# Optimization experiments

Measured on AMD Instinct MI355X. Metric: run time of the kernel, lower is better.

Reference implementation:

```python
import jax, jax.numpy as jnp
import numpy as np

N = 250000   # num nodes
E = 250000   # num edges (tree: ~one parent per node)
D = 128      # embed_size
H = 256      # MLP hidden
HOPS = 3


def _mlp(x, w1, b1, w2, b2):
    # Sequential(Linear, ReLU, Linear, ReLU, Dropout(eval=identity))
    return jax.nn.relu(jnp.dot(jax.nn.relu(jnp.dot(x, w1) + b1), w2) + b2)


def _scatter_mean(src, idx, n):
    s = jax.ops.segment_sum(src, idx, num_segments=n)
    c = jax.ops.segment_sum(jnp.ones((src.shape[0],), src.dtype), idx, num_segments=n)
    return s / jnp.maximum(c, 1.0)[:, None]


def setup_inputs() -> dict:
    key = jax.random.key(0)
    ks = jax.random.split(key, 32)
    u = lambda k, shp: jax.random.uniform(k, shp, jnp.float32, -0.1, 0.1)
    inp = {
        "batch_token": jax.random.normal(ks[0], (N, D), jnp.float32),
        "self_idx_batch": jax.random.randint(ks[1], (E,), 0, N),
        "parent_idx_batch": jax.random.randint(ks[2], (E,), 0, N),
        "root_mask": (jax.random.uniform(ks[3], (N,)) < 0.01).astype(jnp.float32),
        "leaf_mask": (jax.random.uniform(ks[4], (N,)) < 0.3).astype(jnp.float32),
        "start_token": jax.random.normal(ks[5], (D,), jnp.float32),
        "end_token": jax.random.normal(ks[6], (D,), jnp.float32),
        # MLP_V: D -> H -> D
        "Vw1": u(ks[7], (D, H)), "Vb1": u(ks[8], (H,)), "Vw2": u(ks[9], (H, D)), "Vb2": u(ks[10], (D,)),
        # MLP_E: 1 -> H -> D
        "Ew1": u(ks[11], (1, H)), "Eb1": u(ks[12], (H,)), "Ew2": u(ks[13], (H, D)), "Eb2": u(ks[14], (D,)),
        # MLP_p: 3D -> H -> D
        "Pw1": u(ks[15], (3 * D, H)), "Pb1": u(ks[16], (H,)), "Pw2": u(ks[17], (H, D)), "Pb2": u(ks[18], (D,)),
        # MLP_c: 3D -> H -> D
        "Cw1": u(ks[19], (3 * D, H)), "Cb1": u(ks[20], (H,)), "Cw2": u(ks[21], (H, D)), "Cb2": u(ks[22], (D,)),
        # MLP_aggr: 3D -> H -> D
        "Aw1": u(ks[23], (3 * D, H)), "Ab1": u(ks[24], (H,)), "Aw2": u(ks[25], (H, D)), "Ab2": u(ks[26], (D,)),
    }
    return inp


def reference(batch_token, self_idx_batch, parent_idx_batch, root_mask, leaf_mask,
              start_token, end_token,
              Vw1, Vb1, Vw2, Vb2,
              Ew1, Eb1, Ew2, Eb2,
              Pw1, Pb1, Pw2, Pb2,
              Cw1, Cb1, Cw2, Cb2,
              Aw1, Ab1, Aw2, Ab2):
    n = batch_token.shape[0]
    edge_in = _mlp(jnp.ones((1, 1), batch_token.dtype), Ew1, Eb1, Ew2, Eb2)   # [1,D]
    edge_out = _mlp(jnp.zeros((1, 1), batch_token.dtype), Ew1, Eb1, Ew2, Eb2)  # [1,D]
    e = self_idx_batch.shape[0]
    edge_in = jnp.broadcast_to(edge_in, (e, edge_in.shape[1]))
    edge_out = jnp.broadcast_to(edge_out, (e, edge_out.shape[1]))

    hidden = _mlp(batch_token, Vw1, Vb1, Vw2, Vb2)  # [N,D]
    for _ in range(HOPS):
        node_self = hidden[self_idx_batch]      # [E,D] gather
        node_parent = hidden[parent_idx_batch]  # [E,D] gather
        inp_parent = jnp.concatenate([node_parent, node_self, edge_out], axis=-1)  # [E,3D]
        inp_child = jnp.concatenate([node_self, node_parent, edge_in], axis=-1)    # [E,3D]
        S_p = _mlp(inp_parent, Pw1, Pb1, Pw2, Pb2)
        S_c = _mlp(inp_child, Cw1, Cb1, Cw2, Cb2)
        S_p = _scatter_mean(S_p, self_idx_batch, n)
        S_c = _scatter_mean(S_c, parent_idx_batch, n)
        S_p = S_p + root_mask[:, None] * start_token
        S_c = S_c + leaf_mask[:, None] * end_token
        x_aggr = jnp.concatenate([hidden, S_p, S_c], axis=-1)  # [N,3D]
        hidden = hidden + _mlp(x_aggr, Aw1, Ab1, Aw2, Ab2)
    return hidden
```

## Files before the change

### kernel.cpp

```cpp
#include <hip/hip_runtime.h>

typedef __attribute__((ext_vector_type(8))) short short8;
typedef __attribute__((ext_vector_type(4))) float f32x4;

#define DD 128
#define HH 256

__device__ __forceinline__ unsigned short f2bf(float f) {
  unsigned int u = __float_as_uint(f);
  u += 0x7fffu + ((u >> 16) & 1u);
  return (unsigned short)(u >> 16);
}
__device__ __forceinline__ float bf2f(unsigned short s) {
  return __uint_as_float(((unsigned int)s) << 16);
}
__device__ __forceinline__ f32x4 mfma16(short8 a, short8 b, f32x4 c) {
  return __builtin_amdgcn_mfma_f32_16x16x32_bf16(a, b, c, 0, 0, 0);
}

__global__ void wconv(const float* __restrict__ src, unsigned short* __restrict__ dst,
                      int K, int Nout, int kswap) {
  int id = blockIdx.x * 256 + threadIdx.x;
  if (id >= K * Nout) return;
  int n = id / K, k = id - n * K;
  int ks = k + kswap; if (ks >= K) ks -= K;
  dst[n * K + k] = f2bf(src[(size_t)ks * Nout + n]);
}

__global__ void prep_bias(const float* __restrict__ Ew1, const float* __restrict__ Eb1,
                          const float* __restrict__ Ew2, const float* __restrict__ Eb2,
                          const float* __restrict__ Pw1, const float* __restrict__ Pb1,
                          const float* __restrict__ Cw1, const float* __restrict__ Cb1,
                          float* __restrict__ b1P, float* __restrict__ b1C) {
  __shared__ float h1[HH], h0[HH], ein[DD], eout[DD];
  int t = threadIdx.x;
  h1[t] = fmaxf(Ew1[t] + Eb1[t], 0.f);
  h0[t] = fmaxf(Eb1[t], 0.f);
  __syncthreads();
  if (t < DD) {
    float s1 = Eb2[t], s0 = Eb2[t];
    for (int j = 0; j < HH; ++j) { s1 += h1[j] * Ew2[j * DD + t]; s0 += h0[j] * Ew2[j * DD + t]; }
    ein[t]  = fmaxf(s1, 0.f);
    eout[t] = fmaxf(s0, 0.f);
  }
  __syncthreads();
  float bp = Pb1[t], bc = Cb1[t];
  for (int d = 0; d < DD; ++d) {
    bp += eout[d] * Pw1[(size_t)(256 + d) * HH + t];
    bc += ein[d]  * Cw1[(size_t)(256 + d) * HH + t];
  }
  b1P[t] = bp; b1C[t] = bc;
}

__global__ void count_k(const int* __restrict__ selfI, const int* __restrict__ parI,
                        int* degP, int* degC, int E) {
  int id = blockIdx.x * 256 + threadIdx.x;
  if (id < E) { atomicAdd(&degP[selfI[id]], 1); atomicAdd(&degC[parI[id]], 1); }
}

__global__ void scan1(const int* __restrict__ src, int* __restrict__ dst,
                      int* __restrict__ part, int n) {
  __shared__ int sh[256];
  int t = threadIdx.x;
  int base = blockIdx.x * 1024 + t * 4;
  int v0 = base + 0 < n ? src[base + 0] : 0;
  int v1 = base + 1 < n ? src[base + 1] : 0;
  int v2 = base + 2 < n ? src[base + 2] : 0;
  int v3 = base + 3 < n ? src[base + 3] : 0;
  int tsum = v0 + v1 + v2 + v3;
  sh[t] = tsum;
  __syncthreads();
  for (int off = 1; off < 256; off <<= 1) {
    int y = (t >= off) ? sh[t - off] : 0;
    __syncthreads();
    if (t >= off) sh[t] += y;
    __syncthreads();
  }
  int ex = sh[t] - tsum;
  if (base + 0 < n) dst[base + 0] = ex;
  if (base + 1 < n) dst[base + 1] = ex + v0;
  if (base + 2 < n) dst[base + 2] = ex + v0 + v1;
  if (base + 3 < n) dst[base + 3] = ex + v0 + v1 + v2;
  if (t == 255) part[blockIdx.x] = sh[255];
}

__global__ void scan2(int* __restrict__ part, int m) {
  __shared__ int sh[256];
  int t = threadIdx.x;
  int carry = 0;
  for (int base = 0; base < m; base += 256) {
    int v = (base + t < m) ? part[base + t] : 0;
    sh[t] = v;
    __syncthreads();
    for (int off = 1; off < 256; off <<= 1) {
      int y = (t >= off) ? sh[t - off] : 0;
      __syncthreads();
      if (t >= off) sh[t] += y;
      __syncthreads();
    }
    if (base + t < m) part[base + t] = carry + sh[t] - v;
    int tot = sh[255];
    __syncthreads();
    carry += tot;
  }
}

__global__ void scan3(int* __restrict__ dst, const int* __restrict__ part, int n) {
  int i = blockIdx.x * 256 + threadIdx.x;
  if (i < n) dst[i] += part[i >> 10];
}

__global__ void copy2(const int* __restrict__ a, int* __restrict__ b,
                      const int* __restrict__ c, int* __restrict__ d, int n) {
  int i = blockIdx.x * 256 + threadIdx.x;
  if (i < n) { b[i] = a[i]; d[i] = c[i]; }
}

__global__ void pos_k(const int* __restrict__ selfI, const int* __restrict__ parI,
                      int* curP, int* curC, int* posP, int* posC, int E) {
  int e = blockIdx.x * 256 + threadIdx.x;
  if (e < E) {
    posP[e] = atomicAdd(&curP[selfI[e]], 1);
    posC[e] = atomicAdd(&curC[parI[e]], 1);
  }
}

__global__ __launch_bounds__(512, 4) void v_kernel(
    const float* __restrict__ x, const unsigned short* __restrict__ W1t,
    const unsigned short* __restrict__ W2t, const float* __restrict__ b1,
    const float* __restrict__ b2, float* __restrict__ hidden, int n) {
  __shared__ __align__(16) unsigned short A[64 * 136];
  __shared__ __align__(16) unsigned short O1[64 * 264];
  int t = threadIdx.x;
  int w = t >> 6, lane = t & 63, ln = lane & 15, quad = lane >> 4, qo = quad * 8;
  long tile0 = (long)blockIdx.x * 64;
  int rl = t >> 3, part = t & 7;
  int c0 = part * 16;
  long gr = tile0 + rl;
  const float* src = x + (size_t)(gr < n ? gr : 0) * DD + c0;
  unsigned short* arow = A + rl * 136 + c0;
#pragma unroll
  for (int i = 0; i < 4; ++i) {
    float4 v = *(const float4*)(src + i * 4);
    *(ushort4*)(arow + i * 4) = make_ushort4(f2bf(v.x), f2bf(v.y), f2bf(v.z), f2bf(v.w));
  }
  __syncthreads();
  f32x4 acc[4][2];
#pragma unroll
  for (int m = 0; m < 4; ++m) {
    acc[m][0] = {0.f, 0.f, 0.f, 0.f}; acc[m][1] = {0.f, 0.f, 0.f, 0.f};
  }
#pragma unroll
  for (int kt = 0; kt < 4; ++kt) {
    short8 a[4];
#pragma unroll
    for (int m = 0; m < 4; ++m)
      a[m] = *(const short8*)(A + (m * 16 + ln) * 136 + kt * 32 + qo);
#pragma unroll
    for (int nn = 0; nn < 2; ++nn) {
      short8 b = *(const short8*)(W1t + (size_t)(w * 32 + nn * 16 + ln) * 128 + kt * 32 + qo);
#pragma unroll
      for (int m = 0; m < 4; ++m) acc[m][nn] = mfma16(a[m], b, acc[m][nn]);
    }
  }
#pragma unroll
  for (int nn = 0; nn < 2; ++nn) {
    int col = w * 32 + nn * 16 + ln;
    float bb = b1[col];
#pragma unroll
    for (int m = 0; m < 4; ++m)
#pragma unroll
      for (int r = 0; r < 4; ++r)
        O1[(m * 16 + quad * 4 + r) * 264 + col] = f2bf(fmaxf(acc[m][nn][r] + bb, 0.f));
  }
  __syncthreads();
  f32x4 acc2[4];
#pragma unroll
  for (int m = 0; m < 4; ++m) acc2[m] = {0.f, 0.f, 0.f, 0.f};
#pragma unroll
  for (int kt = 0; kt < 8; ++kt) {
    short8 b = *(const short8*)(W2t + (size_t)(w * 16 + ln) * 256 + kt * 32 + qo);
#pragma unroll
    for (int m = 0; m < 4; ++m) {
      short8 a = *(const short8*)(O1 + (m * 16 + ln) * 264 + kt * 32 + qo);
      acc2[m] = mfma16(a, b, acc2[m]);
    }
  }
  {
    int col = w * 16 + ln;
    float bb = b2[col];
#pragma unroll
    for (int m = 0; m < 4; ++m)
#pragma unroll
      for (int r = 0; r < 4; ++r) {
        long gr2 = tile0 + m * 16 + quad * 4 + r;
        if (gr2 < n) hidden[gr2 * DD + col] = fmaxf(acc2[m][r] + bb, 0.f);
      }
  }
}

__global__ __launch_bounds__(512, 4) void edge_kernel(
    const float* __restrict__ hidden, const int* __restrict__ selfI, const int* __restrict__ parI,
    const int* __restrict__ posP, const int* __restrict__ posC,
    const unsigned short* __restrict__ Pw1t, const unsigned short* __restrict__ Pw2t,
    const unsigned short* __restrict__ Cw1t, const unsigned short* __restrict__ Cw2t,
    const float* __restrict__ b1P, const float* __restrict__ b1C,
    const float* __restrict__ b2P, const float* __restrict__ b2C,
    unsigned short* __restrict__ SpE, unsigned short* __restrict__ ScE, int E) {
  __shared__ __align__(16) unsigned short A[64 * 264];
  __shared__ __align__(16) unsigned short O1[64 * 264];
  int t = threadIdx.x;
  int w = t >> 6, lane = t & 63, ln = lane & 15, quad = lane >> 4, qo = quad * 8;
  long tile0 = (long)blockIdx.x * 64;
  int rl = t >> 3, part = t & 7;
  long ge = tile0 + rl;
  bool vrow = ge < E;
  int si = vrow ? selfI[ge] : 0;
  int pi = vrow ? parI[ge] : 0;
  const float* src = (part < 4) ? (hidden + (size_t)si * DD + part * 32)
                                : (hidden + (size_t)pi * DD + (part - 4) * 32);
  unsigned short* dstA = A + rl * 264 + part * 32;
#pragma unroll
  for (int i = 0; i < 8; ++i) {
    float4 v = *(const float4*)(src + i * 4);
    *(ushort4*)(dstA + i * 4) = make_ushort4(f2bf(v.x), f2bf(v.y), f2bf(v.z), f2bf(v.w));
  }
  __syncthreads();

  f32x4 accP[4][2], accC[4][2];
#pragma unroll
  for (int m = 0; m < 4; ++m) {
    accP[m][0] = {0.f, 0.f, 0.f, 0.f}; accP[m][1] = {0.f, 0.f, 0.f, 0.f};
    accC[m][0] = {0.f, 0.f, 0.f, 0.f}; accC[m][1] = {0.f, 0.f, 0.f, 0.f};
  }
#pragma unroll
  for (int kt = 0; kt < 8; ++kt) {
    short8 a[4];
#pragma unroll
    for (int m = 0; m < 4; ++m)
      a[m] = *(const short8*)(A + (m * 16 + ln) * 264 + kt * 32 + qo);
#pragma unroll
    for (int nn = 0; nn < 2; ++nn) {
      short8 bp = *(const short8*)(Pw1t + (size_t)(w * 32 + nn * 16 + ln) * 256 + kt * 32 + qo);
      short8 bc = *(const short8*)(Cw1t + (size_t)(w * 32 + nn * 16 + ln) * 256 + kt * 32 + qo);
#pragma unroll
      for (int m = 0; m < 4; ++m) {
        accP[m][nn] = mfma16(a[m], bp, accP[m][nn]);
        accC[m][nn] = mfma16(a[m], bc, accC[m][nn]);
      }
    }
  }
  __syncthreads();

#pragma unroll
  for (int mlp = 0; mlp < 2; ++mlp) {
    const unsigned short* W2t = mlp ? Cw2t : Pw2t;
    const float* b1 = mlp ? b1C : b1P;
    const float* b2 = mlp ? b2C : b2P;
    unsigned short* Sout = mlp ? ScE : SpE;
    const int* pos = mlp ? posC : posP;
#pragma unroll
    for (int nn = 0; nn < 2; ++nn) {
      int col = w * 32 + nn * 16 + ln;
      float bb = b1[col];
#pragma unroll
      for (int m = 0; m < 4; ++m)
#pragma unroll
        for (int r = 0; r < 4; ++r) {
          float v = mlp ? accC[m][nn][r] : accP[m][nn][r];
          O1[(m * 16 + quad * 4 + r) * 264 + col] = f2bf(fmaxf(v + bb, 0.f));
        }
    }
    __syncthreads();
    f32x4 acc2[4];
#pragma unroll
    for (int m = 0; m < 4; ++m) acc2[m] = {0.f, 0.f, 0.f, 0.f};
#pragma unroll
    for (int kt = 0; kt < 8; ++kt) {
      short8 b = *(const short8*)(W2t + (size_t)(w * 16 + ln) * 256 + kt * 32 + qo);
#pragma unroll
      for (int m = 0; m < 4; ++m) {
        short8 a = *(const short8*)(O1 + (m * 16 + ln) * 264 + kt * 32 + qo);
        acc2[m] = mfma16(a, b, acc2[m]);
      }
    }
    __syncthreads();
    {
      int col = w * 16 + ln;
      float bb = b2[col];
#pragma unroll
      for (int m = 0; m < 4; ++m)
#pragma unroll
        for (int r = 0; r < 4; ++r)
          O1[(m * 16 + quad * 4 + r) * 264 + col] = f2bf(fmaxf(acc2[m][r] + bb, 0.f));
    }
    __syncthreads();
    if (vrow) {
      int dpos = pos[ge];
      const unsigned short* srow = O1 + rl * 264 + part * 16;
      ushort4* dst = (ushort4*)(Sout + (size_t)dpos * DD + part * 16);
#pragma unroll
      for (int i = 0; i < 4; ++i) dst[i] = *(const ushort4*)(srow + i * 4);
    }
    __syncthreads();
  }
}

__global__ __launch_bounds__(512, 4) void node_kernel(
    float* __restrict__ hidden,
    const unsigned short* __restrict__ SpE, const unsigned short* __restrict__ ScE,
    const int* __restrict__ offP, const int* __restrict__ degP,
    const int* __restrict__ offC, const int* __restrict__ degC,
    const float* __restrict__ rootM, const float* __restrict__ leafM,
    const float* __restrict__ startT, const float* __restrict__ endT,
    const unsigned short* __restrict__ W1t, const unsigned short* __restrict__ W2t,
    const float* __restrict__ b1, const float* __restrict__ b2, int n) {
  __shared__ __align__(16) unsigned short A[64 * 392];
  int t = threadIdx.x;
  int w = t >> 6, lane = t & 63, ln = lane & 15, quad = lane >> 4, qo = quad * 8;
  long tile0 = (long)blockIdx.x * 64;
  int rl = t >> 3, part = t & 7;
  int c0 = part * 16;
  long gr = tile0 + rl;
  long g = (gr < n) ? gr : 0;
  unsigned short* arow = A + rl * 392;
  {
    const float* hrow = hidden + (size_t)g * DD + c0;
#pragma unroll
    for (int i = 0; i < 4; ++i) {
      float4 h = *(const float4*)(hrow + i * 4);
      *(ushort4*)(arow + c0 + i * 4) = make_ushort4(f2bf(h.x), f2bf(h.y), f2bf(h.z), f2bf(h.w));
    }
  }
  {
    int off = offP[g], dg = degP[g];
    float s[16];
#pragma unroll
    for (int i = 0; i < 16; ++i) s[i] = 0.f;
    for (int j = 0; j < dg; ++j) {
      const unsigned short* rr = SpE + (size_t)(off + j) * DD + c0;
#pragma unroll
      for (int i = 0; i < 4; ++i) {
        ushort4 u = *(const ushort4*)(rr + i * 4);
        s[i * 4 + 0] += bf2f(u.x); s[i * 4 + 1] += bf2f(u.y);
        s[i * 4 + 2] += bf2f(u.z); s[i * 4 + 3] += bf2f(u.w);
      }
    }
    float ip = 1.f / fmaxf((float)dg, 1.f);
    float rm = rootM[g];
#pragma unroll
    for (int i = 0; i < 4; ++i) {
      float4 st = *(const float4*)(startT + c0 + i * 4);
      *(ushort4*)(arow + 128 + c0 + i * 4) = make_ushort4(
          f2bf(s[i * 4 + 0] * ip + rm * st.x), f2bf(s[i * 4 + 1] * ip + rm * st.y),
          f2bf(s[i * 4 + 2] * ip + rm * st.z), f2bf(s[i * 4 + 3] * ip + rm * st.w));
    }
  }
  {
    int off = offC[g], dg = degC[g];
    float s[16];
#pragma unroll
    for (int i = 0; i < 16; ++i) s[i] = 0.f;
    for (int j = 0; j < dg; ++j) {
      const unsigned short* rr = ScE + (size_t)(off + j) * DD + c0;
#pragma unroll
      for (int i = 0; i < 4; ++i) {
        ushort4 u = *(const ushort4*)(rr + i * 4);
        s[i * 4 + 0] += bf2f(u.x); s[i * 4 + 1] += bf2f(u.y);
        s[i * 4 + 2] += bf2f(u.z); s[i * 4 + 3] += bf2f(u.w);
      }
    }
    float ic = 1.f / fmaxf((float)dg, 1.f);
    float lm = leafM[g];
#pragma unroll
    for (int i = 0; i < 4; ++i) {
      float4 et = *(const float4*)(endT + c0 + i * 4);
      *(ushort4*)(arow + 256 + c0 + i * 4) = make_ushort4(
          f2bf(s[i * 4 + 0] * ic + lm * et.x), f2bf(s[i * 4 + 1] * ic + lm * et.y),
          f2bf(s[i * 4 + 2] * ic + lm * et.z), f2bf(s[i * 4 + 3] * ic + lm * et.w));
    }
  }
  __syncthreads();
  f32x4 acc[4][2];
#pragma unroll
  for (int m = 0; m < 4; ++m) {
    acc[m][0] = {0.f, 0.f, 0.f, 0.f}; acc[m][1] = {0.f, 0.f, 0.f, 0.f};
  }
#pragma unroll
  for (int kt = 0; kt < 12; ++kt) {
    short8 a[4];
#pragma unroll
    for (int m = 0; m < 4; ++m)
      a[m] = *(const short8*)(A + (m * 16 + ln) * 392 + kt * 32 + qo);
#pragma unroll
    for (int nn = 0; nn < 2; ++nn) {
      short8 b = *(const short8*)(W1t + (size_t)(w * 32 + nn * 16 + ln) * 384 + kt * 32 + qo);
#pragma unroll
      for (int m = 0; m < 4; ++m) acc[m][nn] = mfma16(a[m], b, acc[m][nn]);
    }
  }
  __syncthreads();
#pragma unroll
  for (int nn = 0; nn < 2; ++nn) {
    int col = w * 32 + nn * 16 + ln;
    float bb = b1[col];
#pragma unroll
    for (int m = 0; m < 4; ++m)
#pragma unroll
      for (int r = 0; r < 4; ++r)
        A[(m * 16 + quad * 4 + r) * 392 + col] = f2bf(fmaxf(acc[m][nn][r] + bb, 0.f));
  }
  __syncthreads();
  f32x4 acc2[4];
#pragma unroll
  for (int m = 0; m < 4; ++m) acc2[m] = {0.f, 0.f, 0.f, 0.f};
#pragma unroll
  for (int kt = 0; kt < 8; ++kt) {
    short8 b = *(const short8*)(W2t + (size_t)(w * 16 + ln) * 256 + kt * 32 + qo);
#pragma unroll
    for (int m = 0; m < 4; ++m) {
      short8 a = *(const short8*)(A + (m * 16 + ln) * 392 + kt * 32 + qo);
      acc2[m] = mfma16(a, b, acc2[m]);
    }
  }
  __syncthreads();
  {
    int col = w * 16 + ln;
    float bb = b2[col];
#pragma unroll
    for (int m = 0; m < 4; ++m)
#pragma unroll
      for (int r = 0; r < 4; ++r)
        ((float*)(A + (size_t)(m * 16 + quad * 4 + r) * 392))[col] =
            fmaxf(acc2[m][r] + bb, 0.f);
  }
  __syncthreads();
  if (gr < n) {
    const float* F = (const float*)(A + (size_t)rl * 392);
    float* hrow = hidden + (size_t)gr * DD + c0;
#pragma unroll
    for (int i = 0; i < 4; ++i) {
      float4 v = *(const float4*)(F + c0 + i * 4);
      float4 h = *(const float4*)(hrow + i * 4);
      h.x += v.x; h.y += v.y; h.z += v.z; h.w += v.w;
      *(float4*)(hrow + i * 4) = h;
    }
  }
}

extern "C" void kernel_launch(void* const* d_in, const int* in_sizes, int n_in,
                              void* d_out, int out_size, void* d_ws, size_t ws_size,
                              hipStream_t stream) {
  const float* batch  = (const float*)d_in[0];
  const int*   selfI  = (const int*)d_in[1];
  const int*   parI   = (const int*)d_in[2];
  const float* rootM  = (const float*)d_in[3];
  const float* leafM  = (const float*)d_in[4];
  const float* startT = (const float*)d_in[5];
  const float* endT   = (const float*)d_in[6];
  const float* Vw1 = (const float*)d_in[7],  *Vb1 = (const float*)d_in[8];
  const float* Vw2 = (const float*)d_in[9],  *Vb2 = (const float*)d_in[10];
  const float* Ew1 = (const float*)d_in[11], *Eb1 = (const float*)d_in[12];
  const float* Ew2 = (const float*)d_in[13], *Eb2 = (const float*)d_in[14];
  const float* Pw1 = (const float*)d_in[15], *Pb1 = (const float*)d_in[16];
  const float* Pw2 = (const float*)d_in[17], *Pb2 = (const float*)d_in[18];
  const float* Cw1 = (const float*)d_in[19], *Cb1 = (const float*)d_in[20];
  const float* Cw2 = (const float*)d_in[21], *Cb2 = (const float*)d_in[22];
  const float* Aw1 = (const float*)d_in[23], *Ab1 = (const float*)d_in[24];
  const float* Aw2 = (const float*)d_in[25], *Ab2 = (const float*)d_in[26];

  const int N = in_sizes[3];
  const int E = in_sizes[1];
  float* out = (float*)d_out;

  char* p = (char*)d_ws;
  auto nxt = [&](size_t sz) { char* r = p; p += (sz + 255) & ~(size_t)255; return r; };
  unsigned short* SpE = (unsigned short*)nxt((size_t)E * DD * 2);
  unsigned short* ScE = (unsigned short*)nxt((size_t)E * DD * 2);
  int* degP = (int*)nxt((size_t)N * 4);
  int* degC = (int*)nxt((size_t)N * 4);
  int* offP = (int*)nxt((size_t)N * 4);
  int* offC = (int*)nxt((size_t)N * 4);
  int* curP = (int*)nxt((size_t)N * 4);
  int* curC = (int*)nxt((size_t)N * 4);
  int* posP = (int*)nxt((size_t)E * 4);
  int* posC = (int*)nxt((size_t)E * 4);
  int* partA = (int*)nxt(4096);
  int* partB = (int*)nxt(4096);
  unsigned short* Vw1t = (unsigned short*)nxt((size_t)128 * 256 * 2);
  unsigned short* Vw2t = (unsigned short*)nxt((size_t)256 * 128 * 2);
  unsigned short* Pw1t = (unsigned short*)nxt((size_t)256 * 256 * 2);
  unsigned short* Pw2t = (unsigned short*)nxt((size_t)256 * 128 * 2);
  unsigned short* Cw1t = (unsigned short*)nxt((size_t)256 * 256 * 2);
  unsigned short* Cw2t = (unsigned short*)nxt((size_t)256 * 128 * 2);
  unsigned short* Aw1t = (unsigned short*)nxt((size_t)384 * 256 * 2);
  unsigned short* Aw2t = (unsigned short*)nxt((size_t)256 * 128 * 2);
  float* b1P = (float*)nxt(256 * 4);
  float* b1C = (float*)nxt(256 * 4);

  hipMemsetAsync(degP, 0, (size_t)N * 4, stream);
  hipMemsetAsync(degC, 0, (size_t)N * 4, stream);

  auto blk = [](int total) { return dim3((total + 255) / 256); };
  wconv<<<blk(128 * 256), 256, 0, stream>>>(Vw1, Vw1t, 128, 256, 0);
  wconv<<<blk(256 * 128), 256, 0, stream>>>(Vw2, Vw2t, 256, 128, 0);
  wconv<<<blk(256 * 256), 256, 0, stream>>>(Pw1, Pw1t, 256, 256, 128);
  wconv<<<blk(256 * 128), 256, 0, stream>>>(Pw2, Pw2t, 256, 128, 0);
  wconv<<<blk(256 * 256), 256, 0, stream>>>(Cw1, Cw1t, 256, 256, 0);
  wconv<<<blk(256 * 128), 256, 0, stream>>>(Cw2, Cw2t, 256, 128, 0);
  wconv<<<blk(384 * 256), 256, 0, stream>>>(Aw1, Aw1t, 384, 256, 0);
  wconv<<<blk(256 * 128), 256, 0, stream>>>(Aw2, Aw2t, 256, 128, 0);

  prep_bias<<<1, 256, 0, stream>>>(Ew1, Eb1, Ew2, Eb2, Pw1, Pb1, Cw1, Cb1, b1P, b1C);
  count_k<<<blk(E), 256, 0, stream>>>(selfI, parI, degP, degC, E);

  int NB = (N + 1023) / 1024;
  scan1<<<NB, 256, 0, stream>>>(degP, offP, partA, N);
  scan1<<<NB, 256, 0, stream>>>(degC, offC, partB, N);
  scan2<<<1, 256, 0, stream>>>(partA, NB);
  scan2<<<1, 256, 0, stream>>>(partB, NB);
  scan3<<<blk(N), 256, 0, stream>>>(offP, partA, N);
  scan3<<<blk(N), 256, 0, stream>>>(offC, partB, N);
  copy2<<<blk(N), 256, 0, stream>>>(offP, curP, offC, curC, N);
  pos_k<<<blk(E), 256, 0, stream>>>(selfI, parI, curP, curC, posP, posC, E);

  dim3 gN((N + 63) / 64), gE((E + 63) / 64);
  v_kernel<<<gN, 512, 0, stream>>>(batch, Vw1t, Vw2t, Vb1, Vb2, out, N);

  for (int hop = 0; hop < 3; ++hop) {
    edge_kernel<<<gE, 512, 0, stream>>>(out, selfI, parI, posP, posC,
                                        Pw1t, Pw2t, Cw1t, Cw2t, b1P, b1C, Pb2, Cb2,
                                        SpE, ScE, E);
    node_kernel<<<gN, 512, 0, stream>>>(out, SpE, ScE, offP, degP, offC, degC,
                                        rootM, leafM, startT, endT,
                                        Aw1t, Aw2t, Ab1, Ab2, N);
  }
}
```

Before: 1.834 ms.

## Shrink MLP tiles to 32 rows with 4 waves and scatter edge outputs directly

All three MLP kernels now process 32 rows per block with 256 threads (4 waves), so each wave covers 64 hidden columns and 32 output columns, cutting LDS per block and doubling grid size. The edge kernel preloads the scatter positions into shared memory and writes second-layer outputs straight from registers to their sorted positions. This removes the LDS staging round trip and several barriers. In exchange it issues scalar 2-byte global stores instead of vectorized row copies, and weight fragments are reloaded per 32-row tile, doubling weight traffic.

```diff
diff --git a/kernel.cpp b/kernel.cpp
--- a/kernel.cpp
+++ b/kernel.cpp
@@ -125,15 +125,15 @@
   }
 }
 
-__global__ __launch_bounds__(512, 4) void v_kernel(
+__global__ __launch_bounds__(256, 4) void v_kernel(
     const float* __restrict__ x, const unsigned short* __restrict__ W1t,
     const unsigned short* __restrict__ W2t, const float* __restrict__ b1,
     const float* __restrict__ b2, float* __restrict__ hidden, int n) {
-  __shared__ __align__(16) unsigned short A[64 * 136];
-  __shared__ __align__(16) unsigned short O1[64 * 264];
+  __shared__ __align__(16) unsigned short A[32 * 136];
+  __shared__ __align__(16) unsigned short O1[32 * 264];
   int t = threadIdx.x;
   int w = t >> 6, lane = t & 63, ln = lane & 15, quad = lane >> 4, qo = quad * 8;
-  long tile0 = (long)blockIdx.x * 64;
+  long tile0 = (long)blockIdx.x * 32;
   int rl = t >> 3, part = t & 7;
   int c0 = part * 16;
   long gr = tile0 + rl;
@@ -145,61 +145,66 @@
     *(ushort4*)(arow + i * 4) = make_ushort4(f2bf(v.x), f2bf(v.y), f2bf(v.z), f2bf(v.w));
   }
   __syncthreads();
-  f32x4 acc[4][2];
-#pragma unroll
-  for (int m = 0; m < 4; ++m) {
-    acc[m][0] = {0.f, 0.f, 0.f, 0.f}; acc[m][1] = {0.f, 0.f, 0.f, 0.f};
-  }
+  f32x4 acc[2][4];
+#pragma unroll
+  for (int m = 0; m < 2; ++m)
+#pragma unroll
+    for (int nn = 0; nn < 4; ++nn) acc[m][nn] = {0.f, 0.f, 0.f, 0.f};
 #pragma unroll
   for (int kt = 0; kt < 4; ++kt) {
-    short8 a[4];
-#pragma unroll
-    for (int m = 0; m < 4; ++m)
+    short8 a[2];
+#pragma unroll
+    for (int m = 0; m < 2; ++m)
       a[m] = *(const short8*)(A + (m * 16 + ln) * 136 + kt * 32 + qo);
 #pragma unroll
+    for (int nn = 0; nn < 4; ++nn) {
+      short8 b = *(const short8*)(W1t + (size_t)(w * 64 + nn * 16 + ln) * 128 + kt * 32 + qo);
+#pragma unroll
+      for (int m = 0; m < 2; ++m) acc[m][nn] = mfma16(a[m], b, acc[m][nn]);
+    }
+  }
+#pragma unroll
+  for (int nn = 0; nn < 4; ++nn) {
+    int col = w * 64 + nn * 16 + ln;
+    float bb = b1[col];
+#pragma unroll
+    for (int m = 0; m < 2; ++m)
+#pragma unroll
+      for (int r = 0; r < 4; ++r)
+        O1[(m * 16 + quad * 4 + r) * 264 + col] = f2bf(fmaxf(acc[m][nn][r] + bb, 0.f));
+  }
+  __syncthreads();
+  f32x4 acc2[2][2];
+#pragma unroll
+  for (int m = 0; m < 2; ++m) { acc2[m][0] = {0.f, 0.f, 0.f, 0.f}; acc2[m][1] = {0.f, 0.f, 0.f, 0.f}; }
+#pragma unroll
+  for (int kt = 0; kt < 8; ++kt) {
+    short8 a2[2];
+#pragma unroll
+    for (int m = 0; m < 2; ++m)
+      a2[m] = *(const short8*)(O1 + (m * 16 + ln) * 264 + kt * 32 + qo);
+#pragma unroll
     for (int nn = 0; nn < 2; ++nn) {
-      short8 b = *(const short8*)(W1t + (size_t)(w * 32 + nn * 16 + ln) * 128 + kt * 32 + qo);
-#pragma unroll
-      for (int m = 0; m < 4; ++m) acc[m][nn] = mfma16(a[m], b, acc[m][nn]);
+      short8 b = *(const short8*)(W2t + (size_t)(w * 32 + nn * 16 + ln) * 256 + kt * 32 + qo);
+#pragma unroll
+      for (int m = 0; m < 2; ++m) acc2[m][nn] = mfma16(a2[m], b, acc2[m][nn]);
     }
   }
 #pragma unroll
   for (int nn = 0; nn < 2; ++nn) {
     int col = w * 32 + nn * 16 + ln;
-    float bb = b1[col];
-#pragma unroll
-    for (int m = 0; m < 4; ++m)
-#pragma unroll
-      for (int r = 0; r < 4; ++r)
-        O1[(m * 16 + quad * 4 + r) * 264 + col] = f2bf(fmaxf(acc[m][nn][r] + bb, 0.f));
-  }
-  __syncthreads();
-  f32x4 acc2[4];
-#pragma unroll
-  for (int m = 0; m < 4; ++m) acc2[m] = {0.f, 0.f, 0.f, 0.f};
-#pragma unroll
-  for (int kt = 0; kt < 8; ++kt) {
-    short8 b = *(const short8*)(W2t + (size_t)(w * 16 + ln) * 256 + kt * 32 + qo);
-#pragma unroll
-    for (int m = 0; m < 4; ++m) {
-      short8 a = *(const short8*)(O1 + (m * 16 + ln) * 264 + kt * 32 + qo);
-      acc2[m] = mfma16(a, b, acc2[m]);
-    }
-  }
-  {
-    int col = w * 16 + ln;
     float bb = b2[col];
 #pragma unroll
-    for (int m = 0; m < 4; ++m)
+    for (int m = 0; m < 2; ++m)
 #pragma unroll
       for (int r = 0; r < 4; ++r) {
         long gr2 = tile0 + m * 16 + quad * 4 + r;
-        if (gr2 < n) hidden[gr2 * DD + col] = fmaxf(acc2[m][r] + bb, 0.f);
+        if (gr2 < n) hidden[gr2 * DD + col] = fmaxf(acc2[m][nn][r] + bb, 0.f);
       }
   }
 }
 
-__global__ __launch_bounds__(512, 4) void edge_kernel(
+__global__ __launch_bounds__(256, 4) void edge_kernel(
     const float* __restrict__ hidden, const int* __restrict__ selfI, const int* __restrict__ parI,
     const int* __restrict__ posP, const int* __restrict__ posC,
     const unsigned short* __restrict__ Pw1t, const unsigned short* __restrict__ Pw2t,
@@ -207,16 +212,24 @@
     const float* __restrict__ b1P, const float* __restrict__ b1C,
     const float* __restrict__ b2P, const float* __restrict__ b2C,
     unsigned short* __restrict__ SpE, unsigned short* __restrict__ ScE, int E) {
-  __shared__ __align__(16) unsigned short A[64 * 264];
-  __shared__ __align__(16) unsigned short O1[64 * 264];
+  __shared__ __align__(16) unsigned short A[32 * 264];
+  __shared__ __align__(16) unsigned short O1[32 * 264];
+  __shared__ int posS[2][32];
   int t = threadIdx.x;
   int w = t >> 6, lane = t & 63, ln = lane & 15, quad = lane >> 4, qo = quad * 8;
-  long tile0 = (long)blockIdx.x * 64;
+  long tile0 = (long)blockIdx.x * 32;
   int rl = t >> 3, part = t & 7;
   long ge = tile0 + rl;
   bool vrow = ge < E;
   int si = vrow ? selfI[ge] : 0;
   int pi = vrow ? parI[ge] : 0;
+  if (t < 64) {
+    int rr = t & 31;
+    long gg = tile0 + rr;
+    int v = 0;
+    if (gg < E) v = (t < 32) ? posP[gg] : posC[gg];
+    posS[t >> 5][rr] = v;
+  }
   const float* src = (part < 4) ? (hidden + (size_t)si * DD + part * 32)
                                 : (hidden + (size_t)pi * DD + (part - 4) * 32);
   unsigned short* dstA = A + rl * 264 + part * 32;
@@ -227,30 +240,31 @@
   }
   __syncthreads();
 
-  f32x4 accP[4][2], accC[4][2];
-#pragma unroll
-  for (int m = 0; m < 4; ++m) {
-    accP[m][0] = {0.f, 0.f, 0.f, 0.f}; accP[m][1] = {0.f, 0.f, 0.f, 0.f};
-    accC[m][0] = {0.f, 0.f, 0.f, 0.f}; accC[m][1] = {0.f, 0.f, 0.f, 0.f};
-  }
+  f32x4 accP[2][4], accC[2][4];
+#pragma unroll
+  for (int m = 0; m < 2; ++m)
+#pragma unroll
+    for (int nn = 0; nn < 4; ++nn) {
+      accP[m][nn] = {0.f, 0.f, 0.f, 0.f};
+      accC[m][nn] = {0.f, 0.f, 0.f, 0.f};
+    }
 #pragma unroll
   for (int kt = 0; kt < 8; ++kt) {
-    short8 a[4];
-#pragma unroll
-    for (int m = 0; m < 4; ++m)
+    short8 a[2];
+#pragma unroll
+    for (int m = 0; m < 2; ++m)
       a[m] = *(const short8*)(A + (m * 16 + ln) * 264 + kt * 32 + qo);
 #pragma unroll
-    for (int nn = 0; nn < 2; ++nn) {
-      short8 bp = *(const short8*)(Pw1t + (size_t)(w * 32 + nn * 16 + ln) * 256 + kt * 32 + qo);
-      short8 bc = *(const short8*)(Cw1t + (size_t)(w * 32 + nn * 16 + ln) * 256 + kt * 32 + qo);
-#pragma unroll
-      for (int m = 0; m < 4; ++m) {
+    for (int nn = 0; nn < 4; ++nn) {
+      short8 bp = *(const short8*)(Pw1t + (size_t)(w * 64 + nn * 16 + ln) * 256 + kt * 32 + qo);
+      short8 bc = *(const short8*)(Cw1t + (size_t)(w * 64 + nn * 16 + ln) * 256 + kt * 32 + qo);
+#pragma unroll
+      for (int m = 0; m < 2; ++m) {
         accP[m][nn] = mfma16(a[m], bp, accP[m][nn]);
         accC[m][nn] = mfma16(a[m], bc, accC[m][nn]);
       }
     }
   }
-  __syncthreads();
 
 #pragma unroll
   for (int mlp = 0; mlp < 2; ++mlp) {
@@ -258,13 +272,13 @@
     const float* b1 = mlp ? b1C : b1P;
     const float* b2 = mlp ? b2C : b2P;
     unsigned short* Sout = mlp ? ScE : SpE;
-    const int* pos = mlp ? posC : posP;
-#pragma unroll
-    for (int nn = 0; nn < 2; ++nn) {
-      int col = w * 32 + nn * 16 + ln;
+    if (mlp) __syncthreads();
+#pragma unroll
+    for (int nn = 0; nn < 4; ++nn) {
+      int col = w * 64 + nn * 16 + ln;
       float bb = b1[col];
 #pragma unroll
-      for (int m = 0; m < 4; ++m)
+      for (int m = 0; m < 2; ++m)
 #pragma unroll
         for (int r = 0; r < 4; ++r) {
           float v = mlp ? accC[m][nn][r] : accP[m][nn][r];
@@ -272,41 +286,41 @@
         }
     }
     __syncthreads();
-    f32x4 acc2[4];
-#pragma unroll
-    for (int m = 0; m < 4; ++m) acc2[m] = {0.f, 0.f, 0.f, 0.f};
+    f32x4 acc2[2][2];
+#pragma unroll
+    for (int m = 0; m < 2; ++m) { acc2[m][0] = {0.f, 0.f, 0.f, 0.f}; acc2[m][1] = {0.f, 0.f, 0.f, 0.f}; }
 #pragma unroll
     for (int kt = 0; kt < 8; ++kt) {
-      short8 b = *(const short8*)(W2t + (size_t)(w * 16 + ln) * 256 + kt * 32 + qo);
-#pragma unroll
-      for (int m = 0; m < 4; ++m) {
-        short8 a = *(const short8*)(O1 + (m * 16 + ln) * 264 + kt * 32 + qo);
-        acc2[m] = mfma16(a, b, acc2[m]);
+      short8 a2[2];
+#pragma unroll
+      for (int m = 0; m < 2; ++m)
+        a2[m] = *(const short8*)(O1 + (m * 16 + ln) * 264 + kt * 32 + qo);
+#pragma unroll
+      for (int nn = 0; nn < 2; ++nn) {
+        short8 b = *(const short8*)(W2t + (size_t)(w * 32 + nn * 16 + ln) * 256 + kt * 32 + qo);
+#pragma unroll
+        for (int m = 0; m < 2; ++m) acc2[m][nn] = mfma16(a2[m], b, acc2[m][nn]);
       }
     }
-    __syncthreads();
-    {
-      int col = w * 16 + ln;
+#pragma unroll
+    for (int nn = 0; nn < 2; ++nn) {
+      int col = w * 32 + nn * 16 + ln;
       float bb = b2[col];
 #pragma unroll
-      for (int m = 0; m < 4; ++m)
-#pragma unroll
-        for (int r = 0; r < 4; ++r)
-          O1[(m * 16 + quad * 4 + r) * 264 + col] = f2bf(fmaxf(acc2[m][r] + bb, 0.f));
-    }
-    __syncthreads();
-    if (vrow) {
-      int dpos = pos[ge];
-      const unsigned short* srow = O1 + rl * 264 + part * 16;
-      ushort4* dst = (ushort4*)(Sout + (size_t)dpos * DD + part * 16);
-#pragma unroll
-      for (int i = 0; i < 4; ++i) dst[i] = *(const ushort4*)(srow + i * 4);
-    }
-    __syncthreads();
-  }
-}
-
-__global__ __launch_bounds__(512, 4) void node_kernel(
+      for (int m = 0; m < 2; ++m)
+#pragma unroll
+        for (int r = 0; r < 4; ++r) {
+          int row = m * 16 + quad * 4 + r;
+          if (tile0 + row < E) {
+            int dpos = posS[mlp][row];
+            Sout[(size_t)dpos * DD + col] = f2bf(fmaxf(acc2[m][nn][r] + bb, 0.f));
+          }
+        }
+    }
+  }
+}
+
+__global__ __launch_bounds__(256, 4) void node_kernel(
     float* __restrict__ hidden,
     const unsigned short* __restrict__ SpE, const unsigned short* __restrict__ ScE,
     const int* __restrict__ offP, const int* __restrict__ degP,
@@ -315,10 +329,10 @@
     const float* __restrict__ startT, const float* __restrict__ endT,
     const unsigned short* __restrict__ W1t, const unsigned short* __restrict__ W2t,
     const float* __restrict__ b1, const float* __restrict__ b2, int n) {
-  __shared__ __align__(16) unsigned short A[64 * 392];
+  __shared__ __align__(16) unsigned short A[32 * 392];
   int t = threadIdx.x;
   int w = t >> 6, lane = t & 63, ln = lane & 15, quad = lane >> 4, qo = quad * 8;
-  long tile0 = (long)blockIdx.x * 64;
+  long tile0 = (long)blockIdx.x * 32;
   int rl = t >> 3, part = t & 7;
   int c0 = part * 16;
   long gr = tile0 + rl;
@@ -381,58 +395,63 @@
     }
   }
   __syncthreads();
-  f32x4 acc[4][2];
-#pragma unroll
-  for (int m = 0; m < 4; ++m) {
-    acc[m][0] = {0.f, 0.f, 0.f, 0.f}; acc[m][1] = {0.f, 0.f, 0.f, 0.f};
-  }
+  f32x4 acc[2][4];
+#pragma unroll
+  for (int m = 0; m < 2; ++m)
+#pragma unroll
+    for (int nn = 0; nn < 4; ++nn) acc[m][nn] = {0.f, 0.f, 0.f, 0.f};
 #pragma unroll
   for (int kt = 0; kt < 12; ++kt) {
-    short8 a[4];
-#pragma unroll
-    for (int m = 0; m < 4; ++m)
+    short8 a[2];
+#pragma unroll
+    for (int m = 0; m < 2; ++m)
       a[m] = *(const short8*)(A + (m * 16 + ln) * 392 + kt * 32 + qo);
 #pragma unroll
+    for (int nn = 0; nn < 4; ++nn) {
+      short8 b = *(const short8*)(W1t + (size_t)(w * 64 + nn * 16 + ln) * 384 + kt * 32 + qo);
+#pragma unroll
+      for (int m = 0; m < 2; ++m) acc[m][nn] = mfma16(a[m], b, acc[m][nn]);
+    }
+  }
+  __syncthreads();
+#pragma unroll
+  for (int nn = 0; nn < 4; ++nn) {
+    int col = w * 64 + nn * 16 + ln;
+    float bb = b1[col];
+#pragma unroll
+    for (int m = 0; m < 2; ++m)
+#pragma unroll
+      for (int r = 0; r < 4; ++r)
+        A[(m * 16 + quad * 4 + r) * 392 + col] = f2bf(fmaxf(acc[m][nn][r] + bb, 0.f));
+  }
+  __syncthreads();
+  f32x4 acc2[2][2];
+#pragma unroll
+  for (int m = 0; m < 2; ++m) { acc2[m][0] = {0.f, 0.f, 0.f, 0.f}; acc2[m][1] = {0.f, 0.f, 0.f, 0.f}; }
+#pragma unroll
+  for (int kt = 0; kt < 8; ++kt) {
+    short8 a2[2];
+#pragma unroll
+    for (int m = 0; m < 2; ++m)
+      a2[m] = *(const short8*)(A + (m * 16 + ln) * 392 + kt * 32 + qo);
+#pragma unroll
     for (int nn = 0; nn < 2; ++nn) {
-      short8 b = *(const short8*)(W1t + (size_t)(w * 32 + nn * 16 + ln) * 384 + kt * 32 + qo);
-#pragma unroll
-      for (int m = 0; m < 4; ++m) acc[m][nn] = mfma16(a[m], b, acc[m][nn]);
+      short8 b = *(const short8*)(W2t + (size_t)(w * 32 + nn * 16 + ln) * 256 + kt * 32 + qo);
+#pragma unroll
+      for (int m = 0; m < 2; ++m) acc2[m][nn] = mfma16(a2[m], b, acc2[m][nn]);
     }
   }
   __syncthreads();
 #pragma unroll
   for (int nn = 0; nn < 2; ++nn) {
     int col = w * 32 + nn * 16 + ln;
-    float bb = b1[col];
-#pragma unroll
-    for (int m = 0; m < 4; ++m)
-#pragma unroll
-      for (int r = 0; r < 4; ++r)
-        A[(m * 16 + quad * 4 + r) * 392 + col] = f2bf(fmaxf(acc[m][nn][r] + bb, 0.f));
-  }
-  __syncthreads();
-  f32x4 acc2[4];
-#pragma unroll
-  for (int m = 0; m < 4; ++m) acc2[m] = {0.f, 0.f, 0.f, 0.f};
-#pragma unroll
-  for (int kt = 0; kt < 8; ++kt) {
-    short8 b = *(const short8*)(W2t + (size_t)(w * 16 + ln) * 256 + kt * 32 + qo);
-#pragma unroll
-    for (int m = 0; m < 4; ++m) {
-      short8 a = *(const short8*)(A + (m * 16 + ln) * 392 + kt * 32 + qo);
-      acc2[m] = mfma16(a, b, acc2[m]);
-    }
-  }
-  __syncthreads();
-  {
-    int col = w * 16 + ln;
     float bb = b2[col];
 #pragma unroll
-    for (int m = 0; m < 4; ++m)
+    for (int m = 0; m < 2; ++m)
 #pragma unroll
       for (int r = 0; r < 4; ++r)
         ((float*)(A + (size_t)(m * 16 + quad * 4 + r) * 392))[col] =
-            fmaxf(acc2[m][r] + bb, 0.f);
+            fmaxf(acc2[m][nn][r] + bb, 0.f);
   }
   __syncthreads();
   if (gr < n) {
@@ -524,14 +543,14 @@
   copy2<<<blk(N), 256, 0, stream>>>(offP, curP, offC, curC, N);
   pos_k<<<blk(E), 256, 0, stream>>>(selfI, parI, curP, curC, posP, posC, E);
 
-  dim3 gN((N + 63) / 64), gE((E + 63) / 64);
-  v_kernel<<<gN, 512, 0, stream>>>(batch, Vw1t, Vw2t, Vb1, Vb2, out, N);
+  dim3 gN((N + 31) / 32), gE((E + 31) / 32);
+  v_kernel<<<gN, 256, 0, stream>>>(batch, Vw1t, Vw2t, Vb1, Vb2, out, N);
 
   for (int hop = 0; hop < 3; ++hop) {
-    edge_kernel<<<gE, 512, 0, stream>>>(out, selfI, parI, posP, posC,
+    edge_kernel<<<gE, 256, 0, stream>>>(out, selfI, parI, posP, posC,
                                         Pw1t, Pw2t, Cw1t, Cw2t, b1P, b1C, Pb2, Cb2,
                                         SpE, ScE, E);
-    node_kernel<<<gN, 512, 0, stream>>>(out, SpE, ScE, offP, degP, offC, degC,
+    node_kernel<<<gN, 256, 0, stream>>>(out, SpE, ScE, offP, degP, offC, degC,
                                         rootM, leafM, startT, endT,
                                         Aw1t, Aw2t, Ab1, Ab2, N);
   }
```

After: 2.597 ms. +41.6%, slower.
